# Kernel optimization log

Hardware: AMD Instinct MI355X
Metric: run time of the kernel (lower is better)

The kernel has to match this reference:

```python
import jax, jax.numpy as jnp
import numpy as np

B, S, H, NH, HD, FF = 2, 2048, 2048, 16, 128, 8192
EPS = 1e-05
THETA = 10000.0


def _rms(x, w):
    return x * jax.lax.rsqrt(jnp.mean(x * x, axis=-1, keepdims=True) + EPS) * w


def _rope(q, k):
    # q,k: [b, h, s, d]; standard rotate-half RoPE with positions 0..s-1
    s, hd = q.shape[2], q.shape[3]
    inv = 1.0 / (THETA ** (jnp.arange(0, hd, 2, dtype=jnp.float32) / hd))
    f = jnp.arange(s, dtype=jnp.float32)[:, None] * inv[None, :]   # [s, d/2]
    cos = jnp.concatenate([jnp.cos(f), jnp.cos(f)], axis=-1)       # [s, d]
    sin = jnp.concatenate([jnp.sin(f), jnp.sin(f)], axis=-1)
    rot = lambda x: jnp.concatenate([-x[..., hd // 2:], x[..., :hd // 2]], axis=-1)
    return q * cos + rot(q) * sin, k * cos + rot(k) * sin


def _highway(x, w, g, gb):
    # sigmoid(W_g x + b) * (W_h x)
    return jax.nn.sigmoid(x @ g.T + gb) * (x @ w.T)


def setup_inputs() -> dict:
    key = jax.random.key(0)
    ks = jax.random.split(key, 16)
    n = lambda i, shape, s=0.02: jax.random.normal(ks[i], shape, dtype=jnp.float32) * s
    return dict(
        x_mod=n(0, (B, S, H), 1.0),
        x_back=n(1, (B, S, H), 1.0),
        mask=jnp.zeros((1, 1, S, S), jnp.float32),
        wq=n(2, (H, H)), wk=n(3, (H, H)), wv=n(4, (H, H)), wo=n(5, (H, H)),
        cross_ln_w=jnp.ones((H,), jnp.float32),
        fb_w=n(6, (H, H)), fb_g=n(7, (H, H)), fb_gb=jnp.zeros((H,), jnp.float32),
        dr_w=n(8, (H, H)), dr_g=n(9, (H, H)), dr_gb=jnp.zeros((H,), jnp.float32),
        in_ln_w=jnp.ones((H,), jnp.float32),
        post_ln_w=jnp.ones((H,), jnp.float32),
        w_gate=n(10, (FF, H)), w_up=n(11, (FF, H)), w_down=n(12, (H, FF)),
    )


def reference(x_mod, x_back, mask, wq, wk, wv, wo, cross_ln_w,
              fb_w, fb_g, fb_gb, dr_w, dr_g, dr_gb,
              in_ln_w, post_ln_w, w_gate, w_up, w_down):
    b, s, _ = x_mod.shape
    scale = HD ** -0.5

    # feedback highway on x_mod (returned as delta)
    delta = _highway(x_mod, fb_w, fb_g, fb_gb)

    # cross-attention: q from RMSNorm(x_mod), k/v from x_back
    qn = _rms(x_mod, cross_ln_w)
    split = lambda t: t.reshape(b, s, NH, HD).transpose(0, 2, 1, 3)  # [b,h,s,d]
    qh = split(qn @ wq.T)
    kh = split(x_back @ wk.T)
    vh = split(x_back @ wv.T)
    qh, kh = _rope(qh, kh)

    attn = jnp.einsum('bhqd,bhkd->bhqk', qh, kh) * scale + mask
    attn = jax.nn.softmax(attn, axis=-1)  # dropout is identity in eval
    out = jnp.einsum('bhqk,bhkd->bhqd', attn, vh)
    out = out.transpose(0, 2, 1, 3).reshape(b, s, NH * HD)
    mod = out @ wo.T

    # driver highway on x_back
    drv = _highway(x_back, dr_w, dr_g, dr_gb)

    x = x_mod + mod + drv

    # delegated LLaMA-style decoder layer with self_attn == Identity:
    # x = x + Identity(RMSNorm(x)); then x = x + SwiGLU_MLP(RMSNorm(x))
    x = x + _rms(x, in_ln_w)
    h = _rms(x, post_ln_w)
    mlp = (jax.nn.silu(h @ w_gate.T) * (h @ w_up.T)) @ w_down.T
    x = x + mlp

    return (x, delta)
```

## Files before the change

### kernel.cpp

```cpp
#include <hip/hip_runtime.h>
#include <cstdint>
#include <cstddef>

#define H_DIM 2048
#define S_LEN 2048
#define B_SZ  2
#define NH_N  16
#define HD_D  128
#define FF_D  8192
#define T_TOK (B_SZ * S_LEN)
#define MB (size_t)(1 << 20)

typedef __bf16 bf16x8 __attribute__((ext_vector_type(8)));
typedef float  f32x4  __attribute__((ext_vector_type(4)));

__device__ __forceinline__ float bf2f(unsigned short u) {
  unsigned int x = ((unsigned int)u) << 16;
  float f;
  __builtin_memcpy(&f, &x, 4);
  return f;
}
__device__ __forceinline__ unsigned short f2bf(float f) {
  unsigned int x;
  __builtin_memcpy(&x, &f, 4);
  x += 0x7fffu + ((x >> 16) & 1u);
  return (unsigned short)(x >> 16);
}
__device__ __forceinline__ f32x4 mfma16(bf16x8 a, bf16x8 b, f32x4 c) {
  return __builtin_amdgcn_mfma_f32_16x16x32_bf16(a, b, c, 0, 0, 0);
}
__device__ __forceinline__ bf16x8 lds8(const unsigned short* p) {
  return *reinterpret_cast<const bf16x8*>(p);
}
__device__ __forceinline__ void gll16(const unsigned short* g, unsigned short* l) {
  __builtin_amdgcn_global_load_lds(
      (__attribute__((address_space(1))) unsigned int*)(g),
      (__attribute__((address_space(3))) unsigned int*)(l), 16, 0, 0);
}
__device__ __forceinline__ float sigm(float x) { return 1.0f / (1.0f + __expf(-x)); }

__global__ __launch_bounds__(256) void cast_k(const float* __restrict__ in,
                                              unsigned short* __restrict__ o, int n8) {
  const int i = blockIdx.x * 256 + threadIdx.x;
  if (i >= n8) return;
  const size_t base = (size_t)i * 8;
  const float4* p = reinterpret_cast<const float4*>(in + base);
  float4 a = p[0], b = p[1];
  unsigned short ov[8];
  ov[0] = f2bf(a.x); ov[1] = f2bf(a.y); ov[2] = f2bf(a.z); ov[3] = f2bf(a.w);
  ov[4] = f2bf(b.x); ov[5] = f2bf(b.y); ov[6] = f2bf(b.z); ov[7] = f2bf(b.w);
  *reinterpret_cast<uint4*>(o + base) = *(const uint4*)ov;
}

template <int MODE>
__global__ __launch_bounds__(256, 2) void gemm_bt(
    const unsigned short* __restrict__ A, const unsigned short* __restrict__ W,
    void* __restrict__ Cv, const float* __restrict__ Add, int M, int N, int K) {
  __shared__ unsigned short As[128 * 32];
  __shared__ unsigned short Bs[128 * 32];

  const int t    = threadIdx.x;
  const int lane = t & 63;
  const int wave = t >> 6;
  const int lr   = lane & 15;
  const int quad = lane >> 4;
  const int wr   = wave >> 1;
  const int wc   = wave & 1;
  const int row0 = blockIdx.y * 128;
  const int col0 = blockIdx.x * 128;

  const unsigned short* a0 = A + (size_t)(row0 + (t >> 2)) * K + (t & 3) * 8;
  const unsigned short* b0 = W + (size_t)(col0 + (t >> 2)) * K + (t & 3) * 8;
  const size_t k64 = (size_t)64 * K;

  unsigned short* lA0 = &As[t * 8];
  unsigned short* lA1 = &As[2048 + t * 8];
  unsigned short* lB0 = &Bs[t * 8];
  unsigned short* lB1 = &Bs[2048 + t * 8];

  f32x4 acc[4][4];
#pragma unroll
  for (int i = 0; i < 4; ++i)
#pragma unroll
    for (int j = 0; j < 4; ++j) acc[i][j] = (f32x4){0.f, 0.f, 0.f, 0.f};

  for (int kt = 0; kt < K; kt += 32) {
    gll16(a0 + kt, lA0);
    gll16(a0 + kt + k64, lA1);
    gll16(b0 + kt, lB0);
    gll16(b0 + kt + k64, lB1);
    __syncthreads();

    bf16x8 af[4], bfr[4];
#pragma unroll
    for (int i = 0; i < 4; ++i)
      af[i] = lds8(&As[(wr * 64 + i * 16 + lr) * 32 + quad * 8]);
#pragma unroll
    for (int j = 0; j < 4; ++j)
      bfr[j] = lds8(&Bs[(wc * 64 + j * 16 + lr) * 32 + quad * 8]);
#pragma unroll
    for (int i = 0; i < 4; ++i)
#pragma unroll
      for (int j = 0; j < 4; ++j) acc[i][j] = mfma16(af[i], bfr[j], acc[i][j]);
    __syncthreads();
  }

#pragma unroll
  for (int i = 0; i < 4; ++i) {
    const int r0 = row0 + wr * 64 + i * 16 + quad * 4;
#pragma unroll
    for (int j = 0; j < 4; ++j) {
      const int c = col0 + wc * 64 + j * 16 + lr;
      const size_t base = (size_t)r0 * N + c;
      f32x4 v = acc[i][j];
#pragma unroll
      for (int r = 0; r < 4; ++r) {
        if (MODE == 0) {
          ((unsigned short*)Cv)[base + (size_t)r * N] = f2bf(v[r]);
        } else {
          ((float*)Cv)[base + (size_t)r * N] = v[r] + Add[base + (size_t)r * N];
        }
      }
    }
  }
}

template <int OUTBF, int ADDX>
__global__ __launch_bounds__(256) void rms_k(const float* __restrict__ x,
                                             const float* __restrict__ w,
                                             void* __restrict__ o) {
  const int row = blockIdx.x;
  const int t = threadIdx.x;
  const float* xr = x + (size_t)row * H_DIM;

  const float4* xp = reinterpret_cast<const float4*>(xr) + t * 2;
  float4 a = xp[0], b = xp[1];
  float f[8] = {a.x, a.y, a.z, a.w, b.x, b.y, b.z, b.w};
  float ss = 0.f;
#pragma unroll
  for (int m = 0; m < 8; ++m) ss += f[m] * f[m];
#pragma unroll
  for (int off = 32; off > 0; off >>= 1) ss += __shfl_xor(ss, off);
  __shared__ float red[4];
  if ((t & 63) == 0) red[t >> 6] = ss;
  __syncthreads();
  const float tot = red[0] + red[1] + red[2] + red[3];
  const float inv = 1.0f / sqrtf(tot * (1.0f / H_DIM) + 1e-5f);

  const float4* wp = reinterpret_cast<const float4*>(w) + t * 2;
  float4 wa = wp[0], wb = wp[1];
  float wv[8] = {wa.x, wa.y, wa.z, wa.w, wb.x, wb.y, wb.z, wb.w};

  if (OUTBF) {
    unsigned short ov[8];
#pragma unroll
    for (int m = 0; m < 8; ++m) ov[m] = f2bf(f[m] * inv * wv[m]);
    reinterpret_cast<uint4*>((unsigned short*)o + (size_t)row * H_DIM)[t] = *(const uint4*)ov;
  } else {
    float ov[8];
#pragma unroll
    for (int m = 0; m < 8; ++m) {
      float r = f[m] * inv * wv[m];
      ov[m] = ADDX ? (f[m] + r) : r;
    }
    float4* op = reinterpret_cast<float4*>((float*)o + (size_t)row * H_DIM) + t * 2;
    op[0] = *(const float4*)&ov[0];
    op[1] = *(const float4*)&ov[4];
  }
}

__global__ __launch_bounds__(256) void rope_k(unsigned short* __restrict__ q,
                                              unsigned short* __restrict__ k) {
  const int idx  = blockIdx.x * 256 + threadIdx.x;
  const int i    = idx & 63;
  const int head = (idx >> 6) & (NH_N - 1);
  const int tok  = idx >> 10;
  const int pos  = tok & (S_LEN - 1);

  const float inv = expf(-(float)i * (9.210340371976184f / 64.0f));
  const float ang = (float)pos * inv;
  const float c = cosf(ang), s = sinf(ang);

  const size_t base = (size_t)tok * H_DIM + head * HD_D;
  float q1 = bf2f(q[base + i]),      q2 = bf2f(q[base + i + 64]);
  float k1 = bf2f(k[base + i]),      k2 = bf2f(k[base + i + 64]);
  q[base + i]      = f2bf(q1 * c - q2 * s);
  q[base + i + 64] = f2bf(q2 * c + q1 * s);
  k[base + i]      = f2bf(k1 * c - k2 * s);
  k[base + i + 64] = f2bf(k2 * c + k1 * s);
}

__global__ __launch_bounds__(256, 2) void attn_k(const unsigned short* __restrict__ q,
                                                 const unsigned short* __restrict__ kk,
                                                 const unsigned short* __restrict__ vv,
                                                 unsigned short* __restrict__ o) {
  const int bh = blockIdx.y;
  const int b = bh >> 4, h = bh & 15;
  const int q0 = blockIdx.x * 64;
  const int t = threadIdx.x;
  const int lane = t & 63, wave = t >> 6;
  const int lr = lane & 15, quad = lane >> 4;
  const float scale = 0.08838834764831845f;

  __shared__ unsigned short Ks[2][64 * 128];
  __shared__ unsigned short VT[2][128 * 64];
  __shared__ unsigned short Pw[4][16 * 64];

  const size_t qrow = (size_t)(b * S_LEN + q0 + wave * 16 + lr);
  const unsigned short* qbase = q + qrow * H_DIM + h * HD_D;
  bf16x8 qf[4];
#pragma unroll
  for (int c = 0; c < 4; ++c)
    qf[c] = *reinterpret_cast<const bf16x8*>(qbase + c * 32 + quad * 8);

  f32x4 accO[8];
#pragma unroll
  for (int d = 0; d < 8; ++d) accO[d] = (f32x4){0.f, 0.f, 0.f, 0.f};
  float mrow[4] = {-1e30f, -1e30f, -1e30f, -1e30f};
  float lrow[4] = {0.f, 0.f, 0.f, 0.f};

  const unsigned short* kbase = kk + (size_t)(b * S_LEN) * H_DIM + h * HD_D;
  const unsigned short* vbase = vv + (size_t)(b * S_LEN) * H_DIM + h * HD_D;

  uint4 vpre[4];
#pragma unroll
  for (int it = 0; it < 4; ++it) {
    const int idx = it * 256 + t;
    const int key = idx >> 4;
    const int d0  = (idx & 15) * 8;
    gll16(kbase + (size_t)key * H_DIM + (d0 ^ ((key & 7) << 3)), &Ks[0][(size_t)idx * 8]);
    vpre[it] = *reinterpret_cast<const uint4*>(vbase + (size_t)key * H_DIM + d0);
  }

  for (int kv = 0; kv < S_LEN; kv += 64) {
    const int cur = (kv >> 6) & 1;

#pragma unroll
    for (int it = 0; it < 4; ++it) {
      const int idx = it * 256 + t;
      const int key = idx >> 4;
      const int d0  = (idx & 15) * 8;
      const unsigned short* vp = (const unsigned short*)&vpre[it];
#pragma unroll
      for (int m = 0; m < 8; ++m) {
        const int row = d0 + m;
        const int sw  = (row ^ (row >> 3)) & 7;
        *(unsigned short*)((char*)VT[cur] + row * 128 + ((key * 2) ^ (sw << 4))) = vp[m];
      }
    }

    const int nkv = kv + 64;
    if (nkv < S_LEN) {
#pragma unroll
      for (int it = 0; it < 4; ++it) {
        const int idx = it * 256 + t;
        const int key = idx >> 4;
        const int d0  = (idx & 15) * 8;
        gll16(kbase + (size_t)(nkv + key) * H_DIM + (d0 ^ ((key & 7) << 3)),
              &Ks[cur ^ 1][(size_t)idx * 8]);
        vpre[it] = *reinterpret_cast<const uint4*>(
            vbase + (size_t)(nkv + key) * H_DIM + d0);
      }
    }

    asm volatile("s_waitcnt lgkmcnt(0)" ::: "memory");
    __builtin_amdgcn_s_barrier();

    f32x4 sc[4];
#pragma unroll
    for (int kt = 0; kt < 4; ++kt) sc[kt] = (f32x4){0.f, 0.f, 0.f, 0.f};
    __builtin_amdgcn_s_setprio(1);
#pragma unroll
    for (int kt = 0; kt < 4; ++kt)
#pragma unroll
      for (int c = 0; c < 4; ++c) {
        const int row = kt * 16 + lr;
        bf16x8 bfr = *(const bf16x8*)((const char*)Ks[cur] + row * 256 +
                                      ((c * 64 + quad * 16) ^ ((row & 7) << 4)));
        sc[kt] = mfma16(qf[c], bfr, sc[kt]);
      }
    __builtin_amdgcn_s_setprio(0);

    float alpha[4];
#pragma unroll
    for (int r = 0; r < 4; ++r) {
      float mx = fmaxf(fmaxf(sc[0][r], sc[1][r]), fmaxf(sc[2][r], sc[3][r]));
      mx *= scale;
#pragma unroll
      for (int off = 1; off < 16; off <<= 1) mx = fmaxf(mx, __shfl_xor(mx, off));
      const float mnew = fmaxf(mrow[r], mx);
      alpha[r] = __expf(mrow[r] - mnew);
      const int prow = quad * 4 + r;
      const int psw  = (prow ^ (prow >> 3)) & 7;
      float sum = 0.f;
#pragma unroll
      for (int kt = 0; kt < 4; ++kt) {
        float p = __expf(sc[kt][r] * scale - mnew);
        *(unsigned short*)((char*)Pw[wave] + prow * 128 +
                           (((kt * 16 + lr) * 2) ^ (psw << 4))) = f2bf(p);
        sum += p;
      }
#pragma unroll
      for (int off = 1; off < 16; off <<= 1) sum += __shfl_xor(sum, off);
      lrow[r] = lrow[r] * alpha[r] + sum;
      mrow[r] = mnew;
    }
#pragma unroll
    for (int d = 0; d < 8; ++d)
#pragma unroll
      for (int r = 0; r < 4; ++r) accO[d][r] *= alpha[r];

    bf16x8 ap[2];
#pragma unroll
    for (int c = 0; c < 2; ++c)
      ap[c] = *(const bf16x8*)((const char*)Pw[wave] + lr * 128 +
                               ((c * 64 + quad * 16) ^ (((lr ^ (lr >> 3)) & 7) << 4)));
    __builtin_amdgcn_s_setprio(1);
#pragma unroll
    for (int dt = 0; dt < 8; ++dt)
#pragma unroll
      for (int c = 0; c < 2; ++c) {
        const int row = dt * 16 + lr;
        const int sw  = (row ^ (row >> 3)) & 7;
        bf16x8 bfr = *(const bf16x8*)((const char*)VT[cur] + row * 128 +
                                      ((c * 64 + quad * 16) ^ (sw << 4)));
        accO[dt] = mfma16(ap[c], bfr, accO[dt]);
      }
    __builtin_amdgcn_s_setprio(0);

    asm volatile("s_waitcnt lgkmcnt(0)" ::: "memory");
    __builtin_amdgcn_s_barrier();
  }

#pragma unroll
  for (int r = 0; r < 4; ++r) {
    const float invl = 1.0f / lrow[r];
    const size_t orow = (size_t)(b * S_LEN + q0 + wave * 16 + quad * 4 + r);
#pragma unroll
    for (int dt = 0; dt < 8; ++dt)
      o[orow * H_DIM + h * HD_D + dt * 16 + lr] = f2bf(accO[dt][r] * invl);
  }
}

__global__ __launch_bounds__(256) void highway_k(const unsigned short* __restrict__ G,
                                                 const unsigned short* __restrict__ Wx,
                                                 const float* __restrict__ gb,
                                                 float* __restrict__ o) {
  const size_t i8 = (size_t)blockIdx.x * 256 + threadIdx.x;
  const size_t base = i8 * 8;
  const int col = (int)(base & (H_DIM - 1));
  uint4 gv = *reinterpret_cast<const uint4*>(G + base);
  uint4 wv = *reinterpret_cast<const uint4*>(Wx + base);
  const float4* bp = reinterpret_cast<const float4*>(gb + col);
  float4 b0 = bp[0], b1 = bp[1];
  float bb[8] = {b0.x, b0.y, b0.z, b0.w, b1.x, b1.y, b1.z, b1.w};
  const unsigned short *ge = (const unsigned short*)&gv, *we = (const unsigned short*)&wv;
  float ov[8];
#pragma unroll
  for (int m = 0; m < 8; ++m)
    ov[m] = sigm(bf2f(ge[m]) + bb[m]) * bf2f(we[m]);
  float4* op = reinterpret_cast<float4*>(o + base);
  op[0] = *(const float4*)&ov[0];
  op[1] = *(const float4*)&ov[4];
}

__global__ __launch_bounds__(256) void combine_k(const float* __restrict__ xm,
                                                 const unsigned short* __restrict__ mod,
                                                 const unsigned short* __restrict__ G,
                                                 const unsigned short* __restrict__ Wx,
                                                 const float* __restrict__ gb,
                                                 float* __restrict__ o) {
  const size_t i8 = (size_t)blockIdx.x * 256 + threadIdx.x;
  const size_t base = i8 * 8;
  const int col = (int)(base & (H_DIM - 1));
  const float4* xp = reinterpret_cast<const float4*>(xm + base);
  float4 x0 = xp[0], x1 = xp[1];
  float xx[8] = {x0.x, x0.y, x0.z, x0.w, x1.x, x1.y, x1.z, x1.w};
  uint4 mv = *reinterpret_cast<const uint4*>(mod + base);
  uint4 gv = *reinterpret_cast<const uint4*>(G + base);
  uint4 wv = *reinterpret_cast<const uint4*>(Wx + base);
  const float4* bp = reinterpret_cast<const float4*>(gb + col);
  float4 b0 = bp[0], b1 = bp[1];
  float bb[8] = {b0.x, b0.y, b0.z, b0.w, b1.x, b1.y, b1.z, b1.w};
  const unsigned short *me = (const unsigned short*)&mv, *ge = (const unsigned short*)&gv,
                       *we = (const unsigned short*)&wv;
  float ov[8];
#pragma unroll
  for (int m = 0; m < 8; ++m) {
    float drv = sigm(bf2f(ge[m]) + bb[m]) * bf2f(we[m]);
    ov[m] = xx[m] + bf2f(me[m]) + drv;
  }
  float4* op = reinterpret_cast<float4*>(o + base);
  op[0] = *(const float4*)&ov[0];
  op[1] = *(const float4*)&ov[4];
}

__global__ __launch_bounds__(256) void silumul_k(const unsigned short* __restrict__ G,
                                                 const unsigned short* __restrict__ U,
                                                 unsigned short* __restrict__ o) {
  const size_t i8 = (size_t)blockIdx.x * 256 + threadIdx.x;
  const size_t base = i8 * 8;
  uint4 gv = *reinterpret_cast<const uint4*>(G + base);
  uint4 uv = *reinterpret_cast<const uint4*>(U + base);
  const unsigned short *ge = (const unsigned short*)&gv, *ue = (const unsigned short*)&uv;
  unsigned short ov[8];
#pragma unroll
  for (int m = 0; m < 8; ++m) {
    float g = bf2f(ge[m]);
    ov[m] = f2bf(g * sigm(g) * bf2f(ue[m]));
  }
  *reinterpret_cast<uint4*>(o + base) = *(const uint4*)ov;
}

static inline void cast_f2b(const float* in, unsigned short* o, size_t n, hipStream_t st) {
  int n8 = (int)(n / 8);
  cast_k<<<(n8 + 255) / 256, 256, 0, st>>>(in, o, n8);
}
static inline void launch_gemm(const void* A, const void* W, void* C,
                               int M, int N, int K, hipStream_t st) {
  dim3 grid(N / 128, M / 128), blk(256);
  gemm_bt<0><<<grid, blk, 0, st>>>((const unsigned short*)A, (const unsigned short*)W,
                                   C, nullptr, M, N, K);
}

extern "C" void kernel_launch(void* const* d_in, const int* in_sizes, int n_in,
                              void* d_out, int out_size, void* d_ws, size_t ws_size,
                              hipStream_t stream) {
  const float* x_mod      = (const float*)d_in[0];
  const float* x_back     = (const float*)d_in[1];
  const float* wq         = (const float*)d_in[3];
  const float* wk         = (const float*)d_in[4];
  const float* wv         = (const float*)d_in[5];
  const float* wo         = (const float*)d_in[6];
  const float* cross_ln_w = (const float*)d_in[7];
  const float* fb_w       = (const float*)d_in[8];
  const float* fb_g       = (const float*)d_in[9];
  const float* fb_gb      = (const float*)d_in[10];
  const float* dr_w       = (const float*)d_in[11];
  const float* dr_g       = (const float*)d_in[12];
  const float* dr_gb      = (const float*)d_in[13];
  const float* in_ln_w    = (const float*)d_in[14];
  const float* post_ln_w  = (const float*)d_in[15];
  const float* w_gate     = (const float*)d_in[16];
  const float* w_up       = (const float*)d_in[17];
  const float* w_down     = (const float*)d_in[18];

  float* out = (float*)d_out;

  char* w = (char*)d_ws;
  unsigned short* xb0 = (unsigned short*)(w);
  unsigned short* xb1 = (unsigned short*)(w + 16 * MB);
  unsigned short* wb[8];
  for (int i = 0; i < 8; ++i) wb[i] = (unsigned short*)(w + 32 * MB + (size_t)i * 8 * MB);
  unsigned short* wgb = (unsigned short*)(w + 96 * MB);
  unsigned short* wub = (unsigned short*)(w + 128 * MB);
  unsigned short* wdb = (unsigned short*)(w + 160 * MB);
  unsigned short* s0  = (unsigned short*)(w + 192 * MB);
  unsigned short* s1  = (unsigned short*)(w + 208 * MB);
  unsigned short* s2  = (unsigned short*)(w + 224 * MB);
  unsigned short* s3  = (unsigned short*)(w + 240 * MB);
  float*          xf  = (float*)(w + 256 * MB);
  float*          x2f = (float*)(w + 288 * MB);
  unsigned short* f0  = (unsigned short*)(w + 320 * MB);
  unsigned short* f1  = (unsigned short*)(w + 32 * MB);

  const size_t HH = (size_t)H_DIM * H_DIM;
  const size_t FH = (size_t)FF_D * H_DIM;
  const size_t TH = (size_t)T_TOK * H_DIM;

  cast_f2b(x_mod,  xb0,  TH, stream);
  cast_f2b(x_back, xb1,  TH, stream);
  cast_f2b(fb_g,   wb[0], HH, stream);
  cast_f2b(fb_w,   wb[1], HH, stream);
  cast_f2b(wq,     wb[2], HH, stream);
  cast_f2b(wk,     wb[3], HH, stream);
  cast_f2b(wv,     wb[4], HH, stream);
  cast_f2b(wo,     wb[5], HH, stream);
  cast_f2b(dr_g,   wb[6], HH, stream);
  cast_f2b(dr_w,   wb[7], HH, stream);
  cast_f2b(w_gate, wgb,  FH, stream);
  cast_f2b(w_up,   wub,  FH, stream);
  cast_f2b(w_down, wdb,  FH, stream);

  const int ETH = (int)(TH / 8 / 256);
  const int EFF = (int)((size_t)T_TOK * FF_D / 8 / 256);

  launch_gemm(xb0, wb[0], s0, T_TOK, H_DIM, H_DIM, stream);
  launch_gemm(xb0, wb[1], s1, T_TOK, H_DIM, H_DIM, stream);
  highway_k<<<ETH, 256, 0, stream>>>(s0, s1, fb_gb, out + TH);

  rms_k<1, 0><<<T_TOK, 256, 0, stream>>>(x_mod, cross_ln_w, s2);
  launch_gemm(s2, wb[2], s0, T_TOK, H_DIM, H_DIM, stream);
  launch_gemm(xb1, wb[3], s1, T_TOK, H_DIM, H_DIM, stream);
  launch_gemm(xb1, wb[4], s3, T_TOK, H_DIM, H_DIM, stream);

  rope_k<<<T_TOK * NH_N * 64 / 256, 256, 0, stream>>>(s0, s1);

  attn_k<<<dim3(S_LEN / 64, B_SZ * NH_N), 256, 0, stream>>>(s0, s1, s3, s2);

  launch_gemm(s2, wb[5], s0, T_TOK, H_DIM, H_DIM, stream);

  launch_gemm(xb1, wb[6], s1, T_TOK, H_DIM, H_DIM, stream);
  launch_gemm(xb1, wb[7], s3, T_TOK, H_DIM, H_DIM, stream);
  combine_k<<<ETH, 256, 0, stream>>>(x_mod, s0, s1, s3, dr_gb, xf);

  rms_k<0, 1><<<T_TOK, 256, 0, stream>>>(xf, in_ln_w, x2f);
  rms_k<1, 0><<<T_TOK, 256, 0, stream>>>(x2f, post_ln_w, s1);

  launch_gemm(s1, wgb, f0, T_TOK, FF_D, H_DIM, stream);
  launch_gemm(s1, wub, f1, T_TOK, FF_D, H_DIM, stream);
  silumul_k<<<EFF, 256, 0, stream>>>(f0, f1, f0);

  gemm_bt<1><<<dim3(H_DIM / 128, T_TOK / 128), 256, 0, stream>>>(
      f0, wdb, out, x2f, T_TOK, H_DIM, FF_D);

  (void)in_sizes; (void)n_in; (void)out_size; (void)ws_size;
}
```

Measured before the change: 1.666 ms.

## Triple-buffer GEMM loads and fuse highway and SwiGLU epilogues into GEMMs

The GEMM kernel moves to a 3-stage LDS ring with prefetch two tiles ahead, explicit vmcnt waits and raised priority around the MFMA block, and occupancy hint raised to 3. New epilogue modes let the second highway GEMM and the up-projection GEMM read the gate result and apply sigmoid or SiLU-multiply directly, removing two elementwise kernels and their intermediate buffers. This adds LDS use (24KB per block) and reads the aux tensor in the epilogue, where the per-element stores are scattered.

```diff
diff --git a/kernel.cpp b/kernel.cpp
--- a/kernel.cpp
+++ b/kernel.cpp
@@ -53,11 +53,12 @@
 }
 
 template <int MODE>
-__global__ __launch_bounds__(256, 2) void gemm_bt(
+__global__ __launch_bounds__(256, 3) void gemm_bt(
     const unsigned short* __restrict__ A, const unsigned short* __restrict__ W,
-    void* __restrict__ Cv, const float* __restrict__ Add, int M, int N, int K) {
-  __shared__ unsigned short As[128 * 32];
-  __shared__ unsigned short Bs[128 * 32];
+    void* __restrict__ Cv, const void* __restrict__ Aux,
+    const float* __restrict__ Bias, int M, int N, int K) {
+  __shared__ unsigned short As[3][128 * 32];
+  __shared__ unsigned short Bs[3][128 * 32];
 
   const int t    = threadIdx.x;
   const int lane = t & 63;
@@ -73,10 +74,12 @@
   const unsigned short* b0 = W + (size_t)(col0 + (t >> 2)) * K + (t & 3) * 8;
   const size_t k64 = (size_t)64 * K;
 
-  unsigned short* lA0 = &As[t * 8];
-  unsigned short* lA1 = &As[2048 + t * 8];
-  unsigned short* lB0 = &Bs[t * 8];
-  unsigned short* lB1 = &Bs[2048 + t * 8];
+  auto issue = [&](int kt, int bi) {
+    gll16(a0 + kt,       &As[bi][t * 8]);
+    gll16(a0 + kt + k64, &As[bi][2048 + t * 8]);
+    gll16(b0 + kt,       &Bs[bi][t * 8]);
+    gll16(b0 + kt + k64, &Bs[bi][2048 + t * 8]);
+  };
 
   f32x4 acc[4][4];
 #pragma unroll
@@ -84,25 +87,38 @@
 #pragma unroll
     for (int j = 0; j < 4; ++j) acc[i][j] = (f32x4){0.f, 0.f, 0.f, 0.f};
 
+  issue(0, 0);
+  if (K > 32) issue(32, 1);
+
+  int buf = 0;
   for (int kt = 0; kt < K; kt += 32) {
-    gll16(a0 + kt, lA0);
-    gll16(a0 + kt + k64, lA1);
-    gll16(b0 + kt, lB0);
-    gll16(b0 + kt + k64, lB1);
-    __syncthreads();
+    if (kt + 64 < K) {
+      issue(kt + 64, buf == 0 ? 2 : (buf - 1));
+      asm volatile("s_waitcnt vmcnt(8)" ::: "memory");
+    } else if (kt + 32 < K) {
+      asm volatile("s_waitcnt vmcnt(4)" ::: "memory");
+    } else {
+      asm volatile("s_waitcnt vmcnt(0)" ::: "memory");
+    }
+    __builtin_amdgcn_s_barrier();
 
     bf16x8 af[4], bfr[4];
 #pragma unroll
     for (int i = 0; i < 4; ++i)
-      af[i] = lds8(&As[(wr * 64 + i * 16 + lr) * 32 + quad * 8]);
+      af[i] = lds8(&As[buf][(wr * 64 + i * 16 + lr) * 32 + quad * 8]);
 #pragma unroll
     for (int j = 0; j < 4; ++j)
-      bfr[j] = lds8(&Bs[(wc * 64 + j * 16 + lr) * 32 + quad * 8]);
+      bfr[j] = lds8(&Bs[buf][(wc * 64 + j * 16 + lr) * 32 + quad * 8]);
+    __builtin_amdgcn_s_setprio(1);
 #pragma unroll
     for (int i = 0; i < 4; ++i)
 #pragma unroll
       for (int j = 0; j < 4; ++j) acc[i][j] = mfma16(af[i], bfr[j], acc[i][j]);
-    __syncthreads();
+    __builtin_amdgcn_s_setprio(0);
+
+    asm volatile("s_waitcnt lgkmcnt(0)" ::: "memory");
+    __builtin_amdgcn_s_barrier();
+    buf = (buf == 2) ? 0 : (buf + 1);
   }
 
 #pragma unroll
@@ -115,10 +131,17 @@
       f32x4 v = acc[i][j];
 #pragma unroll
       for (int r = 0; r < 4; ++r) {
+        const size_t idx = base + (size_t)r * N;
         if (MODE == 0) {
-          ((unsigned short*)Cv)[base + (size_t)r * N] = f2bf(v[r]);
+          ((unsigned short*)Cv)[idx] = f2bf(v[r]);
+        } else if (MODE == 1) {
+          ((float*)Cv)[idx] = v[r] + ((const float*)Aux)[idx];
+        } else if (MODE == 2) {
+          float g = bf2f(((const unsigned short*)Aux)[idx]);
+          ((unsigned short*)Cv)[idx] = f2bf(g * sigm(g) * v[r]);
         } else {
-          ((float*)Cv)[base + (size_t)r * N] = v[r] + Add[base + (size_t)r * N];
+          float g = bf2f(((const unsigned short*)Aux)[idx]) + Bias[c];
+          ((float*)Cv)[idx] = sigm(g) * v[r];
         }
       }
     }
@@ -340,28 +363,6 @@
     for (int dt = 0; dt < 8; ++dt)
       o[orow * H_DIM + h * HD_D + dt * 16 + lr] = f2bf(accO[dt][r] * invl);
   }
-}
-
-__global__ __launch_bounds__(256) void highway_k(const unsigned short* __restrict__ G,
-                                                 const unsigned short* __restrict__ Wx,
-                                                 const float* __restrict__ gb,
-                                                 float* __restrict__ o) {
-  const size_t i8 = (size_t)blockIdx.x * 256 + threadIdx.x;
-  const size_t base = i8 * 8;
-  const int col = (int)(base & (H_DIM - 1));
-  uint4 gv = *reinterpret_cast<const uint4*>(G + base);
-  uint4 wv = *reinterpret_cast<const uint4*>(Wx + base);
-  const float4* bp = reinterpret_cast<const float4*>(gb + col);
-  float4 b0 = bp[0], b1 = bp[1];
-  float bb[8] = {b0.x, b0.y, b0.z, b0.w, b1.x, b1.y, b1.z, b1.w};
-  const unsigned short *ge = (const unsigned short*)&gv, *we = (const unsigned short*)&wv;
-  float ov[8];
-#pragma unroll
-  for (int m = 0; m < 8; ++m)
-    ov[m] = sigm(bf2f(ge[m]) + bb[m]) * bf2f(we[m]);
-  float4* op = reinterpret_cast<float4*>(o + base);
-  op[0] = *(const float4*)&ov[0];
-  op[1] = *(const float4*)&ov[4];
 }
 
 __global__ __launch_bounds__(256) void combine_k(const float* __restrict__ xm,
@@ -395,23 +396,6 @@
   op[1] = *(const float4*)&ov[4];
 }
 
-__global__ __launch_bounds__(256) void silumul_k(const unsigned short* __restrict__ G,
-                                                 const unsigned short* __restrict__ U,
-                                                 unsigned short* __restrict__ o) {
-  const size_t i8 = (size_t)blockIdx.x * 256 + threadIdx.x;
-  const size_t base = i8 * 8;
-  uint4 gv = *reinterpret_cast<const uint4*>(G + base);
-  uint4 uv = *reinterpret_cast<const uint4*>(U + base);
-  const unsigned short *ge = (const unsigned short*)&gv, *ue = (const unsigned short*)&uv;
-  unsigned short ov[8];
-#pragma unroll
-  for (int m = 0; m < 8; ++m) {
-    float g = bf2f(ge[m]);
-    ov[m] = f2bf(g * sigm(g) * bf2f(ue[m]));
-  }
-  *reinterpret_cast<uint4*>(o + base) = *(const uint4*)ov;
-}
-
 static inline void cast_f2b(const float* in, unsigned short* o, size_t n, hipStream_t st) {
   int n8 = (int)(n / 8);
   cast_k<<<(n8 + 255) / 256, 256, 0, st>>>(in, o, n8);
@@ -420,7 +404,7 @@
                                int M, int N, int K, hipStream_t st) {
   dim3 grid(N / 128, M / 128), blk(256);
   gemm_bt<0><<<grid, blk, 0, st>>>((const unsigned short*)A, (const unsigned short*)W,
-                                   C, nullptr, M, N, K);
+                                   C, nullptr, nullptr, M, N, K);
 }
 
 extern "C" void kernel_launch(void* const* d_in, const int* in_sizes, int n_in,
@@ -462,7 +446,6 @@
   float*          xf  = (float*)(w + 256 * MB);
   float*          x2f = (float*)(w + 288 * MB);
   unsigned short* f0  = (unsigned short*)(w + 320 * MB);
-  unsigned short* f1  = (unsigned short*)(w + 32 * MB);
 
   const size_t HH = (size_t)H_DIM * H_DIM;
   const size_t FH = (size_t)FF_D * H_DIM;
@@ -483,11 +466,10 @@
   cast_f2b(w_down, wdb,  FH, stream);
 
   const int ETH = (int)(TH / 8 / 256);
-  const int EFF = (int)((size_t)T_TOK * FF_D / 8 / 256);
 
   launch_gemm(xb0, wb[0], s0, T_TOK, H_DIM, H_DIM, stream);
-  launch_gemm(xb0, wb[1], s1, T_TOK, H_DIM, H_DIM, stream);
-  highway_k<<<ETH, 256, 0, stream>>>(s0, s1, fb_gb, out + TH);
+  gemm_bt<3><<<dim3(H_DIM / 128, T_TOK / 128), 256, 0, stream>>>(
+      xb0, wb[1], out + TH, s0, fb_gb, T_TOK, H_DIM, H_DIM);
 
   rms_k<1, 0><<<T_TOK, 256, 0, stream>>>(x_mod, cross_ln_w, s2);
   launch_gemm(s2, wb[2], s0, T_TOK, H_DIM, H_DIM, stream);
@@ -508,11 +490,11 @@
   rms_k<1, 0><<<T_TOK, 256, 0, stream>>>(x2f, post_ln_w, s1);
 
   launch_gemm(s1, wgb, f0, T_TOK, FF_D, H_DIM, stream);
-  launch_gemm(s1, wub, f1, T_TOK, FF_D, H_DIM, stream);
-  silumul_k<<<EFF, 256, 0, stream>>>(f0, f1, f0);
+  gemm_bt<2><<<dim3(FF_D / 128, T_TOK / 128), 256, 0, stream>>>(
+      s1, wub, f0, f0, nullptr, T_TOK, FF_D, H_DIM);
 
   gemm_bt<1><<<dim3(H_DIM / 128, T_TOK / 128), 256, 0, stream>>>(
-      f0, wdb, out, x2f, T_TOK, H_DIM, FF_D);
+      f0, wdb, out, x2f, nullptr, T_TOK, H_DIM, FF_D);
 
   (void)in_sizes; (void)n_in; (void)out_size; (void)ws_size;
 }
```

Result: no change. 1.674 ms (+0.5%).
